# Optimization experiments

Hardware: AMD Instinct MI355X
Metric: run time of the kernel (lower is better)

Reference implementation:

```python
import jax, jax.numpy as jnp
import numpy as np

HUGE = 1e9  # stand-in for ops.HUGE_INT


def setup_inputs() -> dict:
    key = jax.random.key(0)
    ks = jax.random.split(key, 8)
    B, Q, K = 8, 128, 256
    Dq = Dk = Dv = H = 512
    query = jax.random.normal(ks[0], (B, Q, Dq), dtype=jnp.float32)
    k_ = jax.random.normal(ks[1], (B, K, Dk), dtype=jnp.float32)
    value = jax.random.normal(ks[2], (B, K, Dv), dtype=jnp.float32)
    mask = jax.random.randint(ks[3], (B, K), 0, 2, dtype=jnp.int32)
    # FFN params: linear1 (Dq+Dk -> H, bias), linear2 (H -> 1, no bias)
    W1 = jax.random.normal(ks[4], (Dq + Dk, H), dtype=jnp.float32) * 0.05
    b1 = jax.random.normal(ks[5], (H,), dtype=jnp.float32) * 0.05
    w2 = jax.random.normal(ks[6], (H, 1), dtype=jnp.float32) * 0.05
    return {"query": query, "key": k_, "value": value, "mask": mask,
            "W1": W1, "b1": b1, "w2": w2}


def reference(query, key, value, mask, W1, b1, w2):
    # Additive (FFN) attention. Original tiles query/key into [B, Q*K, Dq+Dk]
    # and applies linear1; concat@W1 is separable, so we project q and k
    # separately and broadcast-add (same math, no tiled concat tensor).
    Dq = query.shape[-1]
    Wq, Wk = W1[:Dq], W1[Dq:]
    q_proj = jnp.einsum('bqd,dh->bqh', query, Wq)   # [B,Q,H]
    k_proj = jnp.einsum('bkd,dh->bkh', key, Wk)     # [B,K,H]
    hidden = jnp.tanh(q_proj[:, :, None, :] + k_proj[:, None, :, :] + b1)  # [B,Q,K,H]
    scores = jnp.einsum('bqkh,h->bqk', hidden, w2[:, 0])  # [B,Q,K]
    # padding mask fill BEFORE scaling, matching the original op order
    scores = jnp.where(mask[:, None, :] != 0, -HUGE, scores)
    scores = scores / jnp.sqrt(jnp.float32(key.shape[-1]))
    attn_weights = jax.nn.softmax(scores, axis=-1)
    attn_vec = jnp.einsum('bqk,bkv->bqv', attn_weights, value)  # dropout=0 at eval
    return attn_vec, attn_weights
```

## Files before the change

### kernel.cpp

```cpp
#include <hip/hip_runtime.h>
#include <hip/hip_bf16.h>

#define B_ 8
#define Q_ 128
#define K_ 256
#define D_ 512
#define TWOLOG2E 2.8853900817779268f
#define SCALE 0.044194173824159216f
#define L2E 1.4426950408889634f
#define MASKVAL (-44194173.824159216f)

typedef __attribute__((ext_vector_type(8))) short frag8;
typedef __attribute__((ext_vector_type(4))) float f32x4;

__device__ __forceinline__ float fexp2(float x) {
  float r;
  asm("v_exp_f32 %0, %1" : "=v"(r) : "v"(x));
  return r;
}
__device__ __forceinline__ float frcp(float x) {
  float r;
  asm("v_rcp_f32 %0, %1" : "=v"(r) : "v"(x));
  return r;
}
__device__ __forceinline__ unsigned short f2bf(float x) {
  unsigned u = __float_as_uint(x);
  unsigned r = u + 0x7FFFu + ((u >> 16) & 1u);
  return (unsigned short)(r >> 16);
}

__global__ __launch_bounds__(256) void prep_kernel(
    const float* __restrict__ query, const float* __restrict__ key,
    const float* __restrict__ W1,
    unsigned short* __restrict__ Xb, unsigned short* __restrict__ WT) {
  const int t = threadIdx.x;
  if (blockIdx.x < 768) {
    const int r = blockIdx.x * 4 + (t >> 6);
    const int col = (t & 63) * 8;
    const float* src = (r < 1024) ? (query + (size_t)r * D_)
                                  : (key + (size_t)(r - 1024) * D_);
    float4 a = *(const float4*)(src + col);
    float4 b = *(const float4*)(src + col + 4);
    union { frag8 f; unsigned short u[8]; } o;
    o.u[0] = f2bf(a.x); o.u[1] = f2bf(a.y); o.u[2] = f2bf(a.z); o.u[3] = f2bf(a.w);
    o.u[4] = f2bf(b.x); o.u[5] = f2bf(b.y); o.u[6] = f2bf(b.z); o.u[7] = f2bf(b.w);
    *(frag8*)(Xb + (size_t)r * D_ + col) = o.f;
  } else {
    const int bi2 = blockIdx.x - 768;
    const int cd = bi2 >> 2;
    const int hrow = (bi2 & 3) * 256 + t;
    const int half = hrow >> 9;
    const int h = hrow & 511;
    const float* src = W1 + ((size_t)(half * 512 + cd * 8)) * D_ + h;
    union { frag8 f; unsigned short u[8]; } o;
#pragma unroll
    for (int j = 0; j < 8; ++j) o.u[j] = f2bf(src[(size_t)j * D_]);
    *(frag8*)(WT + (size_t)hrow * D_ + cd * 8) = o.f;
  }
}

__global__ __launch_bounds__(256) void gemm_kernel(
    const unsigned short* __restrict__ Xb, const unsigned short* __restrict__ WT,
    const float* __restrict__ b1,
    float* __restrict__ qp, float* __restrict__ kpbT) {
  __shared__ short As[64 * 64];
  __shared__ short Bs[64 * 64];
  const int t = threadIdx.x;
  const int m0 = blockIdx.y * 64;
  const int n0 = blockIdx.x * 64;
  const bool is_k = (m0 >= B_ * Q_);

  const int srow = t >> 2;
  const int sc = t & 3;
  const int skey = srow & 7;
  const int wp0 = srow * 64 + ((sc ^ skey) * 8);
  const int wp1 = srow * 64 + (((sc + 4) ^ skey) * 8);
  const unsigned short* gA = Xb + (size_t)(m0 + srow) * D_ + sc * 8;
  const unsigned short* gB = WT + (size_t)((is_k ? 512 : 0) + n0 + srow) * D_ + sc * 8;

  const int l = t & 63;
  const int w = t >> 6;
  const int lr = l & 15;
  const int kg = l >> 4;
  const int rk = lr & 7;
  int aoff[4][2], boff[2];
#pragma unroll
  for (int kk = 0; kk < 2; ++kk) {
    const int cpos = ((kk * 4 + kg) ^ rk) * 8;
#pragma unroll
    for (int mt = 0; mt < 4; ++mt) aoff[mt][kk] = (mt * 16 + lr) * 64 + cpos;
    boff[kk] = (w * 16 + lr) * 64 + cpos;
  }

  f32x4 acc[4];
#pragma unroll
  for (int mt = 0; mt < 4; ++mt) acc[mt] = (f32x4){0.f, 0.f, 0.f, 0.f};

  for (int k0 = 0; k0 < D_; k0 += 64) {
    frag8 a0 = *(const frag8*)(gA + k0);
    frag8 a1 = *(const frag8*)(gA + k0 + 32);
    frag8 b0 = *(const frag8*)(gB + k0);
    frag8 b1v = *(const frag8*)(gB + k0 + 32);
    __syncthreads();
    *(frag8*)(As + wp0) = a0;
    *(frag8*)(As + wp1) = a1;
    *(frag8*)(Bs + wp0) = b0;
    *(frag8*)(Bs + wp1) = b1v;
    __syncthreads();
#pragma unroll
    for (int kk = 0; kk < 2; ++kk) {
      frag8 bf = *(const frag8*)(Bs + boff[kk]);
#pragma unroll
      for (int mt = 0; mt < 4; ++mt) {
        frag8 af = *(const frag8*)(As + aoff[mt][kk]);
        acc[mt] = __builtin_amdgcn_mfma_f32_16x16x32_bf16(af, bf, acc[mt], 0, 0, 0);
      }
    }
  }

  const int col = n0 + w * 16 + lr;
  if (is_k) {
    const float bc = b1[col];
#pragma unroll
    for (int mt = 0; mt < 4; ++mt) {
      const int krow = m0 - B_ * Q_ + mt * 16 + kg * 4;
      const int bb = krow >> 8;
      const int kk = krow & 255;
      float4 v;
      v.x = (acc[mt][0] + bc) * TWOLOG2E;
      v.y = (acc[mt][1] + bc) * TWOLOG2E;
      v.z = (acc[mt][2] + bc) * TWOLOG2E;
      v.w = (acc[mt][3] + bc) * TWOLOG2E;
      *(float4*)&kpbT[((size_t)bb * D_ + col) * K_ + kk] = v;
    }
  } else {
#pragma unroll
    for (int mt = 0; mt < 4; ++mt) {
#pragma unroll
      for (int i = 0; i < 4; ++i) {
        const int row = m0 + mt * 16 + kg * 4 + i;
        qp[(size_t)row * D_ + col] = acc[mt][i] * TWOLOG2E;
      }
    }
  }
}

__global__ __launch_bounds__(1024) void attn_kernel(
    const float* __restrict__ qp, const float* __restrict__ kpbT,
    const float* __restrict__ value, const int* __restrict__ mask,
    const float* __restrict__ w2,
    float* __restrict__ out_vec, float* __restrict__ out_w) {
  __shared__ float smem_p[16 * 256];
  __shared__ float pw[4 * 256];
  const int b = blockIdx.y;
  const int q0 = blockIdx.x * 4;
  const int t = threadIdx.x;
  const int lane = t & 63;
  const int w = __builtin_amdgcn_readfirstlane(t >> 6);
  const int kc = w & 3;
  const int hq = w >> 2;

  {
    const float* pk = kpbT + ((size_t)b * D_ + hq * 128) * K_ + kc * 64 + lane;
    const float* q_0 = qp + (size_t)(b * Q_ + q0 + 0) * D_ + hq * 128;
    const float* q_1 = qp + (size_t)(b * Q_ + q0 + 1) * D_ + hq * 128;
    const float* q_2 = qp + (size_t)(b * Q_ + q0 + 2) * D_ + hq * 128;
    const float* q_3 = qp + (size_t)(b * Q_ + q0 + 3) * D_ + hq * 128;
    const float* w2h = w2 + hq * 128;

    float a0 = 0.f, a1 = 0.f, a2 = 0.f, a3 = 0.f;
    for (int h = 0; h < 128; h += 8) {
      float kv[8];
#pragma unroll
      for (int j = 0; j < 8; ++j) kv[j] = pk[(size_t)(h + j) * K_];
#pragma unroll
      for (int j = 0; j < 8; ++j) {
        const float wv = w2h[h + j];
        const float r0 = frcp(fexp2(q_0[h + j] + kv[j]) + 1.f);
        const float r1 = frcp(fexp2(q_1[h + j] + kv[j]) + 1.f);
        const float r2 = frcp(fexp2(q_2[h + j] + kv[j]) + 1.f);
        const float r3 = frcp(fexp2(q_3[h + j] + kv[j]) + 1.f);
        a0 = fmaf(wv, r0, a0);
        a1 = fmaf(wv, r1, a1);
        a2 = fmaf(wv, r2, a2);
        a3 = fmaf(wv, r3, a3);
      }
    }
    smem_p[w * 256 + 0 * 64 + lane] = a0;
    smem_p[w * 256 + 1 * 64 + lane] = a1;
    smem_p[w * 256 + 2 * 64 + lane] = a2;
    smem_p[w * 256 + 3 * 64 + lane] = a3;
  }
  __syncthreads();

  if (w < 4) {
    float sw = 0.f;
#pragma unroll
    for (int m = 0; m < 8; ++m) sw += w2[lane + 64 * m];
#pragma unroll
    for (int off = 32; off; off >>= 1) sw += __shfl_xor(sw, off);

    float s[4];
#pragma unroll
    for (int r = 0; r < 4; ++r) {
      float p = smem_p[(0 * 4 + r) * 256 + w * 64 + lane] +
                smem_p[(1 * 4 + r) * 256 + w * 64 + lane] +
                smem_p[(2 * 4 + r) * 256 + w * 64 + lane] +
                smem_p[(3 * 4 + r) * 256 + w * 64 + lane];
      const int mk = mask[b * K_ + r * 64 + lane];
      s[r] = mk ? MASKVAL : fmaf(-2.f, p, sw) * SCALE;
    }
    float mx = fmaxf(fmaxf(s[0], s[1]), fmaxf(s[2], s[3]));
#pragma unroll
    for (int off = 32; off; off >>= 1) mx = fmaxf(mx, __shfl_xor(mx, off));
    float e[4], sum = 0.f;
#pragma unroll
    for (int r = 0; r < 4; ++r) {
      e[r] = fexp2((s[r] - mx) * L2E);
      sum += e[r];
    }
#pragma unroll
    for (int off = 32; off; off >>= 1) sum += __shfl_xor(sum, off);
    const float inv = frcp(sum);
    float* ow = out_w + (size_t)(b * Q_ + q0 + w) * K_;
#pragma unroll
    for (int r = 0; r < 4; ++r) {
      const float p = e[r] * inv;
      pw[w * 256 + r * 64 + lane] = p;
      ow[r * 64 + lane] = p;
    }
  }
  __syncthreads();

  const int col = t & 511;
  const int qq = t >> 9;
  float o0 = 0.f, o1 = 0.f;
  const float* vb = value + (size_t)b * K_ * D_;
  for (int k = 0; k < K_; k += 4) {
    const float4 p0 = *(const float4*)&pw[(qq * 2 + 0) * 256 + k];
    const float4 p1 = *(const float4*)&pw[(qq * 2 + 1) * 256 + k];
    const float v0 = vb[(size_t)(k + 0) * D_ + col];
    const float v1 = vb[(size_t)(k + 1) * D_ + col];
    const float v2 = vb[(size_t)(k + 2) * D_ + col];
    const float v3 = vb[(size_t)(k + 3) * D_ + col];
    o0 = fmaf(p0.x, v0, fmaf(p0.y, v1, fmaf(p0.z, v2, fmaf(p0.w, v3, o0))));
    o1 = fmaf(p1.x, v0, fmaf(p1.y, v1, fmaf(p1.z, v2, fmaf(p1.w, v3, o1))));
  }
  out_vec[(size_t)(b * Q_ + q0 + qq * 2 + 0) * D_ + col] = o0;
  out_vec[(size_t)(b * Q_ + q0 + qq * 2 + 1) * D_ + col] = o1;
}

extern "C" void kernel_launch(void* const* d_in, const int* in_sizes, int n_in,
                              void* d_out, int out_size, void* d_ws, size_t ws_size,
                              hipStream_t stream) {
  const float* query = (const float*)d_in[0];
  const float* key   = (const float*)d_in[1];
  const float* value = (const float*)d_in[2];
  const int*   mask  = (const int*)d_in[3];
  const float* W1    = (const float*)d_in[4];
  const float* b1    = (const float*)d_in[5];
  const float* w2    = (const float*)d_in[6];

  float* out_vec = (float*)d_out;
  float* out_w   = out_vec + (size_t)B_ * Q_ * D_;

  float* qp   = (float*)d_ws;
  float* kpbT = qp + (size_t)B_ * Q_ * D_;
  unsigned short* Xb = (unsigned short*)(kpbT + (size_t)B_ * D_ * K_);
  unsigned short* WT = Xb + (size_t)3072 * D_;

  prep_kernel<<<1024, 256, 0, stream>>>(query, key, W1, Xb, WT);
  gemm_kernel<<<dim3(8, 48), 256, 0, stream>>>(Xb, WT, b1, qp, kpbT);
  attn_kernel<<<dim3(Q_ / 4, B_), 1024, 0, stream>>>(qp, kpbT, value, mask, w2,
                                                     out_vec, out_w);
}
```

Baseline: 121.6 us.

## Fuse bf16 conversion and W1 transpose into GEMM, halve M tile

Drops the separate prep kernel that converted query/key/W1 to bf16 and transposed W1. The GEMM now loads fp32 directly, converts to bf16 on the fly and writes transposed, swizzled tiles into shared memory. The M tile shrinks from 64 to 32, doubling the grid to 768 blocks for better occupancy. This removes a kernel launch and a global round-trip of the converted data, at the cost of more global fp32 traffic per block and redundant conversion of W1 across blocks.

```diff
diff --git a/kernel.cpp b/kernel.cpp
--- a/kernel.cpp
+++ b/kernel.cpp
@@ -23,95 +23,91 @@
   asm("v_rcp_f32 %0, %1" : "=v"(r) : "v"(x));
   return r;
 }
+__device__ __forceinline__ unsigned f2bf_u(float x) {
+  unsigned u = __float_as_uint(x);
+  return (u + 0x7FFFu + ((u >> 16) & 1u)) >> 16;
+}
 __device__ __forceinline__ unsigned short f2bf(float x) {
-  unsigned u = __float_as_uint(x);
-  unsigned r = u + 0x7FFFu + ((u >> 16) & 1u);
-  return (unsigned short)(r >> 16);
-}
-
-__global__ __launch_bounds__(256) void prep_kernel(
+  return (unsigned short)f2bf_u(x);
+}
+__device__ __forceinline__ unsigned packbf(float lo, float hi) {
+  return f2bf_u(lo) | (f2bf_u(hi) << 16);
+}
+
+__global__ __launch_bounds__(256) void gemm_kernel(
     const float* __restrict__ query, const float* __restrict__ key,
-    const float* __restrict__ W1,
-    unsigned short* __restrict__ Xb, unsigned short* __restrict__ WT) {
-  const int t = threadIdx.x;
-  if (blockIdx.x < 768) {
-    const int r = blockIdx.x * 4 + (t >> 6);
-    const int col = (t & 63) * 8;
-    const float* src = (r < 1024) ? (query + (size_t)r * D_)
-                                  : (key + (size_t)(r - 1024) * D_);
-    float4 a = *(const float4*)(src + col);
-    float4 b = *(const float4*)(src + col + 4);
-    union { frag8 f; unsigned short u[8]; } o;
-    o.u[0] = f2bf(a.x); o.u[1] = f2bf(a.y); o.u[2] = f2bf(a.z); o.u[3] = f2bf(a.w);
-    o.u[4] = f2bf(b.x); o.u[5] = f2bf(b.y); o.u[6] = f2bf(b.z); o.u[7] = f2bf(b.w);
-    *(frag8*)(Xb + (size_t)r * D_ + col) = o.f;
-  } else {
-    const int bi2 = blockIdx.x - 768;
-    const int cd = bi2 >> 2;
-    const int hrow = (bi2 & 3) * 256 + t;
-    const int half = hrow >> 9;
-    const int h = hrow & 511;
-    const float* src = W1 + ((size_t)(half * 512 + cd * 8)) * D_ + h;
-    union { frag8 f; unsigned short u[8]; } o;
-#pragma unroll
-    for (int j = 0; j < 8; ++j) o.u[j] = f2bf(src[(size_t)j * D_]);
-    *(frag8*)(WT + (size_t)hrow * D_ + cd * 8) = o.f;
-  }
-}
-
-__global__ __launch_bounds__(256) void gemm_kernel(
-    const unsigned short* __restrict__ Xb, const unsigned short* __restrict__ WT,
-    const float* __restrict__ b1,
+    const float* __restrict__ W1, const float* __restrict__ b1,
     float* __restrict__ qp, float* __restrict__ kpbT) {
-  __shared__ short As[64 * 64];
+  __shared__ short As[32 * 64];
   __shared__ short Bs[64 * 64];
   const int t = threadIdx.x;
-  const int m0 = blockIdx.y * 64;
+  const int m0 = blockIdx.y * 32;
   const int n0 = blockIdx.x * 64;
   const bool is_k = (m0 >= B_ * Q_);
-
-  const int srow = t >> 2;
-  const int sc = t & 3;
-  const int skey = srow & 7;
-  const int wp0 = srow * 64 + ((sc ^ skey) * 8);
-  const int wp1 = srow * 64 + (((sc + 4) ^ skey) * 8);
-  const unsigned short* gA = Xb + (size_t)(m0 + srow) * D_ + sc * 8;
-  const unsigned short* gB = WT + (size_t)((is_k ? 512 : 0) + n0 + srow) * D_ + sc * 8;
+  const float* X = is_k ? key : query;
+  const int xrow0 = is_k ? (m0 - B_ * Q_) : m0;
+  const float* Wb = W1 + (is_k ? (size_t)D_ * D_ : 0);
+
+  const int am = t >> 3;
+  const int ac = t & 7;
+  const float* gA = X + (size_t)(xrow0 + am) * D_ + ac * 8;
+  short* aw = As + am * 64 + ((ac ^ (am & 7)) * 8);
+
+  const int bd = (t & 31) * 2;
+  const int bn = t >> 5;
+  const float* gB0 = Wb + (size_t)bd * D_ + n0 + bn * 8;
+  const float* gB1 = gB0 + D_;
+  const int bchunk = bd >> 3;
+  const int bsub = bd & 7;
 
   const int l = t & 63;
   const int w = t >> 6;
   const int lr = l & 15;
   const int kg = l >> 4;
-  const int rk = lr & 7;
-  int aoff[4][2], boff[2];
+  const int key8 = lr & 7;
+  int aoff[2][2], boff[2];
 #pragma unroll
   for (int kk = 0; kk < 2; ++kk) {
-    const int cpos = ((kk * 4 + kg) ^ rk) * 8;
-#pragma unroll
-    for (int mt = 0; mt < 4; ++mt) aoff[mt][kk] = (mt * 16 + lr) * 64 + cpos;
+    const int cpos = ((kg + kk * 4) ^ key8) * 8;
+#pragma unroll
+    for (int mt = 0; mt < 2; ++mt) aoff[mt][kk] = (mt * 16 + lr) * 64 + cpos;
     boff[kk] = (w * 16 + lr) * 64 + cpos;
   }
 
-  f32x4 acc[4];
-#pragma unroll
-  for (int mt = 0; mt < 4; ++mt) acc[mt] = (f32x4){0.f, 0.f, 0.f, 0.f};
+  f32x4 acc[2];
+  acc[0] = (f32x4){0.f, 0.f, 0.f, 0.f};
+  acc[1] = (f32x4){0.f, 0.f, 0.f, 0.f};
 
   for (int k0 = 0; k0 < D_; k0 += 64) {
-    frag8 a0 = *(const frag8*)(gA + k0);
-    frag8 a1 = *(const frag8*)(gA + k0 + 32);
-    frag8 b0 = *(const frag8*)(gB + k0);
-    frag8 b1v = *(const frag8*)(gB + k0 + 32);
+    float4 a0 = *(const float4*)(gA + k0);
+    float4 a1 = *(const float4*)(gA + k0 + 4);
+    const float* p0 = gB0 + (size_t)k0 * D_;
+    const float* p1 = gB1 + (size_t)k0 * D_;
+    float4 b00 = *(const float4*)(p0);
+    float4 b01 = *(const float4*)(p0 + 4);
+    float4 b10 = *(const float4*)(p1);
+    float4 b11 = *(const float4*)(p1 + 4);
     __syncthreads();
-    *(frag8*)(As + wp0) = a0;
-    *(frag8*)(As + wp1) = a1;
-    *(frag8*)(Bs + wp0) = b0;
-    *(frag8*)(Bs + wp1) = b1v;
+    union { frag8 f; unsigned short u[8]; } av;
+    av.u[0] = f2bf(a0.x); av.u[1] = f2bf(a0.y); av.u[2] = f2bf(a0.z); av.u[3] = f2bf(a0.w);
+    av.u[4] = f2bf(a1.x); av.u[5] = f2bf(a1.y); av.u[6] = f2bf(a1.z); av.u[7] = f2bf(a1.w);
+    *(frag8*)aw = av.f;
+    {
+      float r0[8] = {b00.x, b00.y, b00.z, b00.w, b01.x, b01.y, b01.z, b01.w};
+      float r1[8] = {b10.x, b10.y, b10.z, b10.w, b11.x, b11.y, b11.z, b11.w};
+#pragma unroll
+      for (int j = 0; j < 8; ++j) {
+        const int n = bn * 8 + j;
+        const int epos = ((bchunk ^ j) * 8) + bsub;
+        *(unsigned*)(Bs + n * 64 + epos) = packbf(r0[j], r1[j]);
+      }
+    }
     __syncthreads();
 #pragma unroll
     for (int kk = 0; kk < 2; ++kk) {
       frag8 bf = *(const frag8*)(Bs + boff[kk]);
 #pragma unroll
-      for (int mt = 0; mt < 4; ++mt) {
+      for (int mt = 0; mt < 2; ++mt) {
         frag8 af = *(const frag8*)(As + aoff[mt][kk]);
         acc[mt] = __builtin_amdgcn_mfma_f32_16x16x32_bf16(af, bf, acc[mt], 0, 0, 0);
       }
@@ -122,20 +118,20 @@
   if (is_k) {
     const float bc = b1[col];
 #pragma unroll
-    for (int mt = 0; mt < 4; ++mt) {
+    for (int mt = 0; mt < 2; ++mt) {
       const int krow = m0 - B_ * Q_ + mt * 16 + kg * 4;
       const int bb = krow >> 8;
-      const int kk = krow & 255;
+      const int kk0 = krow & 255;
       float4 v;
       v.x = (acc[mt][0] + bc) * TWOLOG2E;
       v.y = (acc[mt][1] + bc) * TWOLOG2E;
       v.z = (acc[mt][2] + bc) * TWOLOG2E;
       v.w = (acc[mt][3] + bc) * TWOLOG2E;
-      *(float4*)&kpbT[((size_t)bb * D_ + col) * K_ + kk] = v;
+      *(float4*)&kpbT[((size_t)bb * D_ + col) * K_ + kk0] = v;
     }
   } else {
 #pragma unroll
-    for (int mt = 0; mt < 4; ++mt) {
+    for (int mt = 0; mt < 2; ++mt) {
 #pragma unroll
       for (int i = 0; i < 4; ++i) {
         const int row = m0 + mt * 16 + kg * 4 + i;
@@ -266,11 +262,8 @@
 
   float* qp   = (float*)d_ws;
   float* kpbT = qp + (size_t)B_ * Q_ * D_;
-  unsigned short* Xb = (unsigned short*)(kpbT + (size_t)B_ * D_ * K_);
-  unsigned short* WT = Xb + (size_t)3072 * D_;
-
-  prep_kernel<<<1024, 256, 0, stream>>>(query, key, W1, Xb, WT);
-  gemm_kernel<<<dim3(8, 48), 256, 0, stream>>>(Xb, WT, b1, qp, kpbT);
+
+  gemm_kernel<<<dim3(8, 96), 256, 0, stream>>>(query, key, W1, b1, qp, kpbT);
   attn_kernel<<<dim3(Q_ / 4, B_), 1024, 0, stream>>>(qp, kpbT, value, mask, w2,
                                                      out_vec, out_w);
 }
```

Result: slower. 128.0 us (+5.2%).
